# Optimization experiments

Measured on AMD Instinct MI355X. Metric: run time of the kernel, lower is better.

The kernel has to match this reference:

```python
import jax, jax.numpy as jnp
import numpy as np

B, C, N = 8, 128, 2048
HEADS = 4
OUT = 128
HD = OUT // HEADS  # 32


def setup_inputs() -> dict:
    key = jax.random.key(0)
    kx, kq, kk, kv, ko = jax.random.split(key, 5)
    # xavier_uniform bounds
    def xavier(k, shape, fan_in, fan_out):
        a = float(np.sqrt(6.0 / (fan_in + fan_out)))
        return jax.random.uniform(k, shape, jnp.float32, -a, a)
    return {
        "x": jax.random.normal(kx, (B, C, N), jnp.float32),
        "W_q": xavier(kq, (HEADS, C, HD), C, HD),
        "W_k": xavier(kk, (HEADS, C, HD), C, HD),
        "W_v": xavier(kv, (HEADS, C, HD), C, HD),
        "W_o": xavier(ko, (OUT, OUT), OUT, OUT),
    }


def reference(x, W_q, W_k, W_v, W_o):
    # x: [B, C, N] -> x_t: [B, N, C]
    x_t = jnp.transpose(x, (0, 2, 1))
    # per-head projections: [B, H, N, d]
    q = jnp.einsum("bnc,hcd->bhnd", x_t, W_q)
    k = jnp.einsum("bnc,hcd->bhnd", x_t, W_k)
    v = jnp.einsum("bnc,hcd->bhnd", x_t, W_v)
    scale = 1.0 / jnp.sqrt(jnp.asarray(HD, jnp.float32))
    # materialized score matrix [B, H, N, N]
    scores = jax.nn.softmax(jnp.einsum("bhnd,bhmd->bhnm", q, k) * scale, axis=-1)
    # weighted sum per head then concat heads: [B, N, H*d]
    out = jnp.einsum("bhnm,bhmd->bhnd", scores, v)
    out = jnp.transpose(out, (0, 2, 1, 3)).reshape(B, N, OUT)
    out = out @ W_o  # [B, N, OUT]
    adj = jnp.mean(scores, axis=1)  # [B, N, N]
    return jnp.transpose(out, (0, 2, 1)), adj
```

## Files before the change

### kernel.cpp

```cpp
#include <hip/hip_runtime.h>
#include <hip/hip_bf16.h>

#define NB 8
#define NC 128
#define NN 2048
#define NH 4
#define HD 32
#define NOUT 128

typedef _Float16 half8 __attribute__((ext_vector_type(8)));
typedef float f32x4 __attribute__((ext_vector_type(4)));

__device__ __forceinline__ f32x4 mfma16(half8 a, half8 b, f32x4 c) {
  return __builtin_amdgcn_mfma_f32_16x16x32_f16(a, b, c, 0, 0, 0);
}

__global__ __launch_bounds__(256) void k_proj(
    const float* __restrict__ x, const float* __restrict__ Wq,
    const float* __restrict__ Wk, const float* __restrict__ Wv,
    _Float16* __restrict__ qo, _Float16* __restrict__ ko, _Float16* __restrict__ vto)
{
  const int bid = blockIdx.x;
  const int b  = bid & 7;
  const int n0 = (bid >> 3) * 64;
  const int h  = threadIdx.x >> 6;
  const int l  = threadIdx.x & 63;
  const int lr = l & 15, lg = l >> 4;

  half8 a[4][4];
#pragma unroll
  for (int rf = 0; rf < 4; ++rf)
#pragma unroll
    for (int kc = 0; kc < 4; ++kc)
#pragma unroll
      for (int j = 0; j < 8; ++j)
        a[rf][kc][j] = (_Float16)x[(size_t)(b*NC + kc*32 + lg*8 + j)*NN + n0 + rf*16 + lr];

#pragma unroll
  for (int m = 0; m < 2; ++m) {
    const float* W = m ? Wk : Wq;
    _Float16* dst  = m ? ko : qo;
    f32x4 acc[4][2] = {};
#pragma unroll
    for (int kc = 0; kc < 4; ++kc) {
      half8 wb[2];
#pragma unroll
      for (int cf = 0; cf < 2; ++cf)
#pragma unroll
        for (int j = 0; j < 8; ++j)
          wb[cf][j] = (_Float16)W[(size_t)(h*NC + kc*32 + lg*8 + j)*HD + cf*16 + lr];
#pragma unroll
      for (int rf = 0; rf < 4; ++rf)
#pragma unroll
        for (int cf = 0; cf < 2; ++cf)
          acc[rf][cf] = mfma16(a[rf][kc], wb[cf], acc[rf][cf]);
    }
#pragma unroll
    for (int rf = 0; rf < 4; ++rf)
#pragma unroll
      for (int cf = 0; cf < 2; ++cf)
#pragma unroll
        for (int r = 0; r < 4; ++r)
          dst[((size_t)(b*NH + h)*NN + n0 + rf*16 + lg*4 + r)*HD + cf*16 + lr] =
              (_Float16)acc[rf][cf][r];
  }

  {
    half8 aw[2][4];
#pragma unroll
    for (int rf = 0; rf < 2; ++rf)
#pragma unroll
      for (int kc = 0; kc < 4; ++kc)
#pragma unroll
        for (int j = 0; j < 8; ++j)
          aw[rf][kc][j] = (_Float16)Wv[(size_t)(h*NC + kc*32 + lg*8 + j)*HD + rf*16 + lr];
    f32x4 acc[2][4] = {};
#pragma unroll
    for (int kc = 0; kc < 4; ++kc)
#pragma unroll
      for (int rf = 0; rf < 2; ++rf)
#pragma unroll
        for (int nf = 0; nf < 4; ++nf)
          acc[rf][nf] = mfma16(aw[rf][kc], a[nf][kc], acc[rf][nf]);
#pragma unroll
    for (int rf = 0; rf < 2; ++rf)
#pragma unroll
      for (int nf = 0; nf < 4; ++nf)
#pragma unroll
        for (int r = 0; r < 4; ++r)
          vto[((size_t)(b*NH + h)*HD + rf*16 + lg*4 + r)*NN + n0 + nf*16 + lr] =
              (_Float16)acc[rf][nf][r];
  }
}

union SMem {
  _Float16 p[NH * 32 * 72];
  struct { _Float16 ocat[32 * 136]; float ot[128 * 36]; } ep;
};

__global__ __launch_bounds__(256) void k_attn(
    const _Float16* __restrict__ q, const _Float16* __restrict__ k,
    const _Float16* __restrict__ vt, const float* __restrict__ Wo,
    float* __restrict__ outT, float* __restrict__ adj)
{
  __shared__ SMem sm;
  const int bid = blockIdx.x;
  const int b  = bid & 7;
  const int n0 = (bid >> 3) * 32;
  const int h  = threadIdx.x >> 6;
  const int l  = threadIdx.x & 63;
  const int lr = l & 15, lg = l >> 4;

  const _Float16* qh = q  + (size_t)(b*NH + h) * NN * HD;
  const _Float16* kh = k  + (size_t)(b*NH + h) * NN * HD;
  const _Float16* vh = vt + (size_t)(b*NH + h) * HD * NN;

  half8 qa[2];
  qa[0] = *(const half8*)(qh + (size_t)(n0 + lr)*HD + lg*8);
  qa[1] = *(const half8*)(qh + (size_t)(n0 + 16 + lr)*HD + lg*8);

  const float c1 = 0.25504527f;
  const float c2 = 17.3123405f;

  float rs[2][4] = {};
  for (int mt = 0; mt < NN/16; ++mt) {
    half8 kb = *(const half8*)(kh + (size_t)(mt*16 + lr)*HD + lg*8);
    f32x4 z{};
    f32x4 s0 = mfma16(qa[0], kb, z);
    f32x4 s1 = mfma16(qa[1], kb, z);
#pragma unroll
    for (int r = 0; r < 4; ++r) {
      rs[0][r] += __builtin_amdgcn_exp2f(s0[r]*c1 - c2);
      rs[1][r] += __builtin_amdgcn_exp2f(s1[r]*c1 - c2);
    }
  }
#pragma unroll
  for (int rf = 0; rf < 2; ++rf)
#pragma unroll
    for (int r = 0; r < 4; ++r) {
      float v = rs[rf][r];
      v += __shfl_xor(v, 1); v += __shfl_xor(v, 2);
      v += __shfl_xor(v, 4); v += __shfl_xor(v, 8);
      rs[rf][r] = 1.0f / v;
    }

  f32x4 oacc[2][2] = {};
  const int tr = threadIdx.x >> 3;
  const int tc = (threadIdx.x & 7) * 8;

  for (int mt2 = 0; mt2 < NN/64; ++mt2) {
#pragma unroll
    for (int st = 0; st < 4; ++st) {
      half8 kb = *(const half8*)(kh + (size_t)(mt2*64 + st*16 + lr)*HD + lg*8);
      f32x4 z{};
      f32x4 s0 = mfma16(qa[0], kb, z);
      f32x4 s1 = mfma16(qa[1], kb, z);
#pragma unroll
      for (int r = 0; r < 4; ++r) {
        sm.p[h*2304 + (lg*4 + r)*72 + st*16 + lr] =
            (_Float16)(__builtin_amdgcn_exp2f(s0[r]*c1 - c2) * rs[0][r]);
        sm.p[h*2304 + (16 + lg*4 + r)*72 + st*16 + lr] =
            (_Float16)(__builtin_amdgcn_exp2f(s1[r]*c1 - c2) * rs[1][r]);
      }
    }
    __syncthreads();
#pragma unroll
    for (int kc = 0; kc < 2; ++kc) {
      half8 pa0 = *(const half8*)(&sm.p[h*2304 + lr*72 + kc*32 + lg*8]);
      half8 pa1 = *(const half8*)(&sm.p[h*2304 + (16 + lr)*72 + kc*32 + lg*8]);
      half8 vb0 = *(const half8*)(vh + (size_t)lr*NN        + mt2*64 + kc*32 + lg*8);
      half8 vb1 = *(const half8*)(vh + (size_t)(16 + lr)*NN + mt2*64 + kc*32 + lg*8);
      oacc[0][0] = mfma16(pa0, vb0, oacc[0][0]);
      oacc[0][1] = mfma16(pa0, vb1, oacc[0][1]);
      oacc[1][0] = mfma16(pa1, vb0, oacc[1][0]);
      oacc[1][1] = mfma16(pa1, vb1, oacc[1][1]);
    }
    {
      float a8[8] = {};
#pragma unroll
      for (int h2 = 0; h2 < 4; ++h2) {
        half8 pv = *(const half8*)(&sm.p[h2*2304 + tr*72 + tc]);
#pragma unroll
        for (int i = 0; i < 8; ++i) a8[i] += (float)pv[i];
      }
      size_t base = ((size_t)(b*NN) + n0 + tr)*NN + mt2*64 + tc;
      f32x4 w0 = {a8[0]*0.25f, a8[1]*0.25f, a8[2]*0.25f, a8[3]*0.25f};
      f32x4 w1 = {a8[4]*0.25f, a8[5]*0.25f, a8[6]*0.25f, a8[7]*0.25f};
      *(f32x4*)(adj + base)     = w0;
      *(f32x4*)(adj + base + 4) = w1;
    }
    __syncthreads();
  }

#pragma unroll
  for (int rf = 0; rf < 2; ++rf)
#pragma unroll
    for (int df = 0; df < 2; ++df)
#pragma unroll
      for (int r = 0; r < 4; ++r)
        sm.ep.ocat[(rf*16 + lg*4 + r)*136 + h*32 + df*16 + lr] = (_Float16)oacc[rf][df][r];
  __syncthreads();

  f32x4 o2[2][2] = {};
#pragma unroll
  for (int kc = 0; kc < 4; ++kc) {
    half8 a2[2];
    a2[0] = *(const half8*)(&sm.ep.ocat[lr*136        + kc*32 + lg*8]);
    a2[1] = *(const half8*)(&sm.ep.ocat[(16 + lr)*136 + kc*32 + lg*8]);
    half8 wb[2];
#pragma unroll
    for (int of = 0; of < 2; ++of)
#pragma unroll
      for (int j = 0; j < 8; ++j)
        wb[of][j] = (_Float16)Wo[(size_t)(kc*32 + lg*8 + j)*NOUT + h*32 + of*16 + lr];
#pragma unroll
    for (int rf = 0; rf < 2; ++rf)
#pragma unroll
      for (int of = 0; of < 2; ++of)
        o2[rf][of] = mfma16(a2[rf], wb[of], o2[rf][of]);
  }
#pragma unroll
  for (int rf = 0; rf < 2; ++rf)
#pragma unroll
    for (int of = 0; of < 2; ++of)
#pragma unroll
      for (int r = 0; r < 4; ++r)
        sm.ep.ot[(h*32 + of*16 + lr)*36 + rf*16 + lg*4 + r] = o2[rf][of][r];
  __syncthreads();
  {
    int o  = threadIdx.x >> 1;
    int nn = (threadIdx.x & 1) * 16;
    float* dst = outT + ((size_t)(b*NOUT) + o)*NN + n0 + nn;
#pragma unroll
    for (int i = 0; i < 4; ++i)
      *(f32x4*)(dst + i*4) = *(const f32x4*)(&sm.ep.ot[o*36 + nn + i*4]);
  }
}

extern "C" void kernel_launch(void* const* d_in, const int* in_sizes, int n_in,
                              void* d_out, int out_size, void* d_ws, size_t ws_size,
                              hipStream_t stream) {
  const float* x  = (const float*)d_in[0];
  const float* Wq = (const float*)d_in[1];
  const float* Wk = (const float*)d_in[2];
  const float* Wv = (const float*)d_in[3];
  const float* Wo = (const float*)d_in[4];

  float* outT = (float*)d_out;
  float* adj  = outT + (size_t)NB * NOUT * NN;

  const size_t qkv_elems = (size_t)NB * NH * NN * HD;
  _Float16* qw = (_Float16*)d_ws;
  _Float16* kw = qw + qkv_elems;
  _Float16* vw = kw + qkv_elems;

  k_proj<<<dim3(NB * (NN/64)), dim3(256), 0, stream>>>(x, Wq, Wk, Wv, qw, kw, vw);
  k_attn<<<dim3(NB * (NN/32)), dim3(256), 0, stream>>>(qw, kw, vw, Wo, outT, adj);
}
```

Before: 260.0 us.

## Halve attention query tile, pre-transpose weights to fp16, stage x via LDS

The attention kernel now processes 16 query rows per block instead of 32, doubling the grid to 1024 blocks for better occupancy and latency hiding. The cost is that K and V are reread twice as often. A new prep kernel converts and transposes all weight matrices to fp16 once, so the projection and output GEMMs can use vector loads instead of strided scalar converts. The projection kernel also stages x through shared memory with coalesced float4 loads and uses smaller 32-column tiles.

```diff
diff --git a/kernel.cpp b/kernel.cpp
--- a/kernel.cpp
+++ b/kernel.cpp
@@ -7,233 +7,234 @@
 #define NH 4
 #define HD 32
 #define NOUT 128
+#define QB 16
 
 typedef _Float16 half8 __attribute__((ext_vector_type(8)));
+typedef _Float16 half4 __attribute__((ext_vector_type(4)));
 typedef float f32x4 __attribute__((ext_vector_type(4)));
 
 __device__ __forceinline__ f32x4 mfma16(half8 a, half8 b, f32x4 c) {
   return __builtin_amdgcn_mfma_f32_16x16x32_f16(a, b, c, 0, 0, 0);
 }
 
+__global__ __launch_bounds__(256) void k_prep(
+    const float* __restrict__ Wq, const float* __restrict__ Wk,
+    const float* __restrict__ Wv, const float* __restrict__ Wo,
+    _Float16* __restrict__ WqT, _Float16* __restrict__ WkT,
+    _Float16* __restrict__ WvT, _Float16* __restrict__ WoT)
+{
+  int id = blockIdx.x * 256 + threadIdx.x;
+  if (id < 3 * 16384) {
+    int m = id >> 14, rem = id & 16383;
+    int h = rem >> 12, d = (rem >> 7) & 31, c = rem & 127;
+    const float* W = (m == 0) ? Wq : (m == 1) ? Wk : Wv;
+    _Float16* WT   = (m == 0) ? WqT : (m == 1) ? WkT : WvT;
+    WT[(h * 32 + d) * 128 + c] = (_Float16)W[(h * 128 + c) * 32 + d];
+  } else {
+    int j = id - 49152;
+    int o = j >> 7, c = j & 127;
+    WoT[o * 128 + c] = (_Float16)Wo[c * 128 + o];
+  }
+}
+
 __global__ __launch_bounds__(256) void k_proj(
-    const float* __restrict__ x, const float* __restrict__ Wq,
-    const float* __restrict__ Wk, const float* __restrict__ Wv,
+    const float* __restrict__ x, const _Float16* __restrict__ WqT,
+    const _Float16* __restrict__ WkT, const _Float16* __restrict__ WvT,
     _Float16* __restrict__ qo, _Float16* __restrict__ ko, _Float16* __restrict__ vto)
 {
+  __shared__ _Float16 xs[32][136];
   const int bid = blockIdx.x;
   const int b  = bid & 7;
-  const int n0 = (bid >> 3) * 64;
-  const int h  = threadIdx.x >> 6;
-  const int l  = threadIdx.x & 63;
-  const int lr = l & 15, lg = l >> 4;
-
-  half8 a[4][4];
-#pragma unroll
-  for (int rf = 0; rf < 4; ++rf)
+  const int n0 = (bid >> 3) * 32;
+  const int tid = threadIdx.x;
+  const int h = tid >> 6, l = tid & 63, lr = l & 15, lg = l >> 4;
+
+  {
+    int c  = tid >> 1;
+    int nq = (tid & 1) * 16;
+    const float* src = x + (size_t)(b * NC + c) * NN + n0 + nq;
+#pragma unroll
+    for (int i = 0; i < 4; ++i) {
+      f32x4 v = *(const f32x4*)(src + i * 4);
+#pragma unroll
+      for (int j = 0; j < 4; ++j) xs[nq + i * 4 + j][c] = (_Float16)v[j];
+    }
+  }
+  __syncthreads();
+
+  half8 a[2][4];
+#pragma unroll
+  for (int rf = 0; rf < 2; ++rf)
 #pragma unroll
     for (int kc = 0; kc < 4; ++kc)
-#pragma unroll
-      for (int j = 0; j < 8; ++j)
-        a[rf][kc][j] = (_Float16)x[(size_t)(b*NC + kc*32 + lg*8 + j)*NN + n0 + rf*16 + lr];
+      a[rf][kc] = *(const half8*)(&xs[rf * 16 + lr][kc * 32 + lg * 8]);
 
 #pragma unroll
   for (int m = 0; m < 2; ++m) {
-    const float* W = m ? Wk : Wq;
-    _Float16* dst  = m ? ko : qo;
-    f32x4 acc[4][2] = {};
+    const _Float16* WT = m ? WkT : WqT;
+    _Float16* dst      = m ? ko : qo;
+    f32x4 acc[2][2] = {};
 #pragma unroll
     for (int kc = 0; kc < 4; ++kc) {
       half8 wb[2];
 #pragma unroll
       for (int cf = 0; cf < 2; ++cf)
-#pragma unroll
-        for (int j = 0; j < 8; ++j)
-          wb[cf][j] = (_Float16)W[(size_t)(h*NC + kc*32 + lg*8 + j)*HD + cf*16 + lr];
-#pragma unroll
-      for (int rf = 0; rf < 4; ++rf)
+        wb[cf] = *(const half8*)(WT + (size_t)(h * HD + cf * 16 + lr) * NC + kc * 32 + lg * 8);
+#pragma unroll
+      for (int rf = 0; rf < 2; ++rf)
 #pragma unroll
         for (int cf = 0; cf < 2; ++cf)
           acc[rf][cf] = mfma16(a[rf][kc], wb[cf], acc[rf][cf]);
     }
 #pragma unroll
-    for (int rf = 0; rf < 4; ++rf)
+    for (int rf = 0; rf < 2; ++rf)
 #pragma unroll
       for (int cf = 0; cf < 2; ++cf)
 #pragma unroll
         for (int r = 0; r < 4; ++r)
-          dst[((size_t)(b*NH + h)*NN + n0 + rf*16 + lg*4 + r)*HD + cf*16 + lr] =
+          dst[((size_t)(b * NH + h) * NN + n0 + rf * 16 + lg * 4 + r) * HD + cf * 16 + lr] =
               (_Float16)acc[rf][cf][r];
   }
 
   {
-    half8 aw[2][4];
+    f32x4 acc[2][2] = {};
+#pragma unroll
+    for (int kc = 0; kc < 4; ++kc) {
+      half8 aw[2];
+#pragma unroll
+      for (int rf = 0; rf < 2; ++rf)
+        aw[rf] = *(const half8*)(WvT + (size_t)(h * HD + rf * 16 + lr) * NC + kc * 32 + lg * 8);
+#pragma unroll
+      for (int rf = 0; rf < 2; ++rf)
+#pragma unroll
+        for (int nf = 0; nf < 2; ++nf)
+          acc[rf][nf] = mfma16(aw[rf], a[nf][kc], acc[rf][nf]);
+    }
 #pragma unroll
     for (int rf = 0; rf < 2; ++rf)
 #pragma unroll
-      for (int kc = 0; kc < 4; ++kc)
-#pragma unroll
-        for (int j = 0; j < 8; ++j)
-          aw[rf][kc][j] = (_Float16)Wv[(size_t)(h*NC + kc*32 + lg*8 + j)*HD + rf*16 + lr];
-    f32x4 acc[2][4] = {};
-#pragma unroll
-    for (int kc = 0; kc < 4; ++kc)
-#pragma unroll
-      for (int rf = 0; rf < 2; ++rf)
-#pragma unroll
-        for (int nf = 0; nf < 4; ++nf)
-          acc[rf][nf] = mfma16(aw[rf][kc], a[nf][kc], acc[rf][nf]);
-#pragma unroll
-    for (int rf = 0; rf < 2; ++rf)
-#pragma unroll
-      for (int nf = 0; nf < 4; ++nf)
+      for (int nf = 0; nf < 2; ++nf)
 #pragma unroll
         for (int r = 0; r < 4; ++r)
-          vto[((size_t)(b*NH + h)*HD + rf*16 + lg*4 + r)*NN + n0 + nf*16 + lr] =
+          vto[((size_t)(b * NH + h) * HD + rf * 16 + lg * 4 + r) * NN + n0 + nf * 16 + lr] =
               (_Float16)acc[rf][nf][r];
   }
 }
 
 union SMem {
-  _Float16 p[NH * 32 * 72];
-  struct { _Float16 ocat[32 * 136]; float ot[128 * 36]; } ep;
+  _Float16 p[NH * QB * 72];
+  struct { _Float16 ocat[QB * 136]; float ot[128 * 20]; } ep;
 };
 
 __global__ __launch_bounds__(256) void k_attn(
     const _Float16* __restrict__ q, const _Float16* __restrict__ k,
-    const _Float16* __restrict__ vt, const float* __restrict__ Wo,
+    const _Float16* __restrict__ vt, const _Float16* __restrict__ WoT,
     float* __restrict__ outT, float* __restrict__ adj)
 {
   __shared__ SMem sm;
   const int bid = blockIdx.x;
   const int b  = bid & 7;
-  const int n0 = (bid >> 3) * 32;
+  const int n0 = (bid >> 3) * QB;
   const int h  = threadIdx.x >> 6;
   const int l  = threadIdx.x & 63;
   const int lr = l & 15, lg = l >> 4;
 
-  const _Float16* qh = q  + (size_t)(b*NH + h) * NN * HD;
-  const _Float16* kh = k  + (size_t)(b*NH + h) * NN * HD;
-  const _Float16* vh = vt + (size_t)(b*NH + h) * HD * NN;
-
-  half8 qa[2];
-  qa[0] = *(const half8*)(qh + (size_t)(n0 + lr)*HD + lg*8);
-  qa[1] = *(const half8*)(qh + (size_t)(n0 + 16 + lr)*HD + lg*8);
+  const _Float16* qh = q  + (size_t)(b * NH + h) * NN * HD;
+  const _Float16* kh = k  + (size_t)(b * NH + h) * NN * HD;
+  const _Float16* vh = vt + (size_t)(b * NH + h) * HD * NN;
+
+  half8 qa = *(const half8*)(qh + (size_t)(n0 + lr) * HD + lg * 8);
 
   const float c1 = 0.25504527f;
   const float c2 = 17.3123405f;
 
-  float rs[2][4] = {};
-  for (int mt = 0; mt < NN/16; ++mt) {
-    half8 kb = *(const half8*)(kh + (size_t)(mt*16 + lr)*HD + lg*8);
+  float rs[4] = {};
+  for (int mt = 0; mt < NN / 32; ++mt) {
+    half8 kb0 = *(const half8*)(kh + (size_t)(mt * 32 + lr) * HD + lg * 8);
+    half8 kb1 = *(const half8*)(kh + (size_t)(mt * 32 + 16 + lr) * HD + lg * 8);
     f32x4 z{};
-    f32x4 s0 = mfma16(qa[0], kb, z);
-    f32x4 s1 = mfma16(qa[1], kb, z);
-#pragma unroll
-    for (int r = 0; r < 4; ++r) {
-      rs[0][r] += __builtin_amdgcn_exp2f(s0[r]*c1 - c2);
-      rs[1][r] += __builtin_amdgcn_exp2f(s1[r]*c1 - c2);
-    }
-  }
-#pragma unroll
-  for (int rf = 0; rf < 2; ++rf)
-#pragma unroll
-    for (int r = 0; r < 4; ++r) {
-      float v = rs[rf][r];
-      v += __shfl_xor(v, 1); v += __shfl_xor(v, 2);
-      v += __shfl_xor(v, 4); v += __shfl_xor(v, 8);
-      rs[rf][r] = 1.0f / v;
-    }
-
-  f32x4 oacc[2][2] = {};
-  const int tr = threadIdx.x >> 3;
-  const int tc = (threadIdx.x & 7) * 8;
-
-  for (int mt2 = 0; mt2 < NN/64; ++mt2) {
+    f32x4 s0 = mfma16(qa, kb0, z);
+    f32x4 s1 = mfma16(qa, kb1, z);
+#pragma unroll
+    for (int r = 0; r < 4; ++r)
+      rs[r] += __builtin_amdgcn_exp2f(s0[r] * c1 - c2) +
+               __builtin_amdgcn_exp2f(s1[r] * c1 - c2);
+  }
+#pragma unroll
+  for (int r = 0; r < 4; ++r) {
+    float v = rs[r];
+    v += __shfl_xor(v, 1); v += __shfl_xor(v, 2);
+    v += __shfl_xor(v, 4); v += __shfl_xor(v, 8);
+    rs[r] = 1.0f / v;
+  }
+
+  f32x4 oacc[2] = {};
+  const int tr = threadIdx.x >> 4;
+  const int tc = (threadIdx.x & 15) * 4;
+
+  for (int mt2 = 0; mt2 < NN / 64; ++mt2) {
 #pragma unroll
     for (int st = 0; st < 4; ++st) {
-      half8 kb = *(const half8*)(kh + (size_t)(mt2*64 + st*16 + lr)*HD + lg*8);
+      half8 kb = *(const half8*)(kh + (size_t)(mt2 * 64 + st * 16 + lr) * HD + lg * 8);
       f32x4 z{};
-      f32x4 s0 = mfma16(qa[0], kb, z);
-      f32x4 s1 = mfma16(qa[1], kb, z);
-#pragma unroll
-      for (int r = 0; r < 4; ++r) {
-        sm.p[h*2304 + (lg*4 + r)*72 + st*16 + lr] =
-            (_Float16)(__builtin_amdgcn_exp2f(s0[r]*c1 - c2) * rs[0][r]);
-        sm.p[h*2304 + (16 + lg*4 + r)*72 + st*16 + lr] =
-            (_Float16)(__builtin_amdgcn_exp2f(s1[r]*c1 - c2) * rs[1][r]);
+      f32x4 s = mfma16(qa, kb, z);
+#pragma unroll
+      for (int r = 0; r < 4; ++r)
+        sm.p[(h * QB + lg * 4 + r) * 72 + st * 16 + lr] =
+            (_Float16)(__builtin_amdgcn_exp2f(s[r] * c1 - c2) * rs[r]);
+    }
+    __syncthreads();
+#pragma unroll
+    for (int kc = 0; kc < 2; ++kc) {
+      half8 pa  = *(const half8*)(&sm.p[(h * QB + lr) * 72 + kc * 32 + lg * 8]);
+      half8 vb0 = *(const half8*)(vh + (size_t)lr * NN        + mt2 * 64 + kc * 32 + lg * 8);
+      half8 vb1 = *(const half8*)(vh + (size_t)(16 + lr) * NN + mt2 * 64 + kc * 32 + lg * 8);
+      oacc[0] = mfma16(pa, vb0, oacc[0]);
+      oacc[1] = mfma16(pa, vb1, oacc[1]);
+    }
+    {
+      float a4[4] = {};
+#pragma unroll
+      for (int h2 = 0; h2 < 4; ++h2) {
+        half4 pv = *(const half4*)(&sm.p[(h2 * QB + tr) * 72 + tc]);
+#pragma unroll
+        for (int i = 0; i < 4; ++i) a4[i] += (float)pv[i];
       }
+      f32x4 w = {a4[0] * 0.25f, a4[1] * 0.25f, a4[2] * 0.25f, a4[3] * 0.25f};
+      *(f32x4*)(adj + ((size_t)(b * NN) + n0 + tr) * NN + mt2 * 64 + tc) = w;
     }
     __syncthreads();
-#pragma unroll
-    for (int kc = 0; kc < 2; ++kc) {
-      half8 pa0 = *(const half8*)(&sm.p[h*2304 + lr*72 + kc*32 + lg*8]);
-      half8 pa1 = *(const half8*)(&sm.p[h*2304 + (16 + lr)*72 + kc*32 + lg*8]);
-      half8 vb0 = *(const half8*)(vh + (size_t)lr*NN        + mt2*64 + kc*32 + lg*8);
-      half8 vb1 = *(const half8*)(vh + (size_t)(16 + lr)*NN + mt2*64 + kc*32 + lg*8);
-      oacc[0][0] = mfma16(pa0, vb0, oacc[0][0]);
-      oacc[0][1] = mfma16(pa0, vb1, oacc[0][1]);
-      oacc[1][0] = mfma16(pa1, vb0, oacc[1][0]);
-      oacc[1][1] = mfma16(pa1, vb1, oacc[1][1]);
-    }
-    {
-      float a8[8] = {};
-#pragma unroll
-      for (int h2 = 0; h2 < 4; ++h2) {
-        half8 pv = *(const half8*)(&sm.p[h2*2304 + tr*72 + tc]);
-#pragma unroll
-        for (int i = 0; i < 8; ++i) a8[i] += (float)pv[i];
-      }
-      size_t base = ((size_t)(b*NN) + n0 + tr)*NN + mt2*64 + tc;
-      f32x4 w0 = {a8[0]*0.25f, a8[1]*0.25f, a8[2]*0.25f, a8[3]*0.25f};
-      f32x4 w1 = {a8[4]*0.25f, a8[5]*0.25f, a8[6]*0.25f, a8[7]*0.25f};
-      *(f32x4*)(adj + base)     = w0;
-      *(f32x4*)(adj + base + 4) = w1;
-    }
-    __syncthreads();
-  }
-
-#pragma unroll
-  for (int rf = 0; rf < 2; ++rf)
-#pragma unroll
-    for (int df = 0; df < 2; ++df)
-#pragma unroll
-      for (int r = 0; r < 4; ++r)
-        sm.ep.ocat[(rf*16 + lg*4 + r)*136 + h*32 + df*16 + lr] = (_Float16)oacc[rf][df][r];
+  }
+
+#pragma unroll
+  for (int df = 0; df < 2; ++df)
+#pragma unroll
+    for (int r = 0; r < 4; ++r)
+      sm.ep.ocat[(lg * 4 + r) * 136 + h * 32 + df * 16 + lr] = (_Float16)oacc[df][r];
   __syncthreads();
 
-  f32x4 o2[2][2] = {};
+  f32x4 o2[2] = {};
 #pragma unroll
   for (int kc = 0; kc < 4; ++kc) {
-    half8 a2[2];
-    a2[0] = *(const half8*)(&sm.ep.ocat[lr*136        + kc*32 + lg*8]);
-    a2[1] = *(const half8*)(&sm.ep.ocat[(16 + lr)*136 + kc*32 + lg*8]);
-    half8 wb[2];
-#pragma unroll
-    for (int of = 0; of < 2; ++of)
-#pragma unroll
-      for (int j = 0; j < 8; ++j)
-        wb[of][j] = (_Float16)Wo[(size_t)(kc*32 + lg*8 + j)*NOUT + h*32 + of*16 + lr];
-#pragma unroll
-    for (int rf = 0; rf < 2; ++rf)
-#pragma unroll
-      for (int of = 0; of < 2; ++of)
-        o2[rf][of] = mfma16(a2[rf], wb[of], o2[rf][of]);
-  }
-#pragma unroll
-  for (int rf = 0; rf < 2; ++rf)
-#pragma unroll
-    for (int of = 0; of < 2; ++of)
-#pragma unroll
-      for (int r = 0; r < 4; ++r)
-        sm.ep.ot[(h*32 + of*16 + lr)*36 + rf*16 + lg*4 + r] = o2[rf][of][r];
+    half8 a2 = *(const half8*)(&sm.ep.ocat[lr * 136 + kc * 32 + lg * 8]);
+#pragma unroll
+    for (int of = 0; of < 2; ++of) {
+      half8 wb = *(const half8*)(WoT + (size_t)(h * 32 + of * 16 + lr) * NOUT + kc * 32 + lg * 8);
+      o2[of] = mfma16(a2, wb, o2[of]);
+    }
+  }
+#pragma unroll
+  for (int of = 0; of < 2; ++of)
+#pragma unroll
+    for (int r = 0; r < 4; ++r)
+      sm.ep.ot[(h * 32 + of * 16 + lr) * 20 + lg * 4 + r] = o2[of][r];
   __syncthreads();
   {
     int o  = threadIdx.x >> 1;
-    int nn = (threadIdx.x & 1) * 16;
-    float* dst = outT + ((size_t)(b*NOUT) + o)*NN + n0 + nn;
-#pragma unroll
-    for (int i = 0; i < 4; ++i)
-      *(f32x4*)(dst + i*4) = *(const f32x4*)(&sm.ep.ot[o*36 + nn + i*4]);
+    int hf = threadIdx.x & 1;
+    float* dst = outT + ((size_t)(b * NOUT) + o) * NN + n0 + hf * 8;
+    *(f32x4*)(dst)     = *(const f32x4*)(&sm.ep.ot[o * 20 + hf * 8]);
+    *(f32x4*)(dst + 4) = *(const f32x4*)(&sm.ep.ot[o * 20 + hf * 8 + 4]);
   }
 }
 
@@ -250,10 +251,15 @@
   float* adj  = outT + (size_t)NB * NOUT * NN;
 
   const size_t qkv_elems = (size_t)NB * NH * NN * HD;
-  _Float16* qw = (_Float16*)d_ws;
-  _Float16* kw = qw + qkv_elems;
-  _Float16* vw = kw + qkv_elems;
-
-  k_proj<<<dim3(NB * (NN/64)), dim3(256), 0, stream>>>(x, Wq, Wk, Wv, qw, kw, vw);
-  k_attn<<<dim3(NB * (NN/32)), dim3(256), 0, stream>>>(qw, kw, vw, Wo, outT, adj);
-}
+  _Float16* qw  = (_Float16*)d_ws;
+  _Float16* kw  = qw + qkv_elems;
+  _Float16* vw  = kw + qkv_elems;
+  _Float16* wqT = vw + qkv_elems;
+  _Float16* wkT = wqT + 16384;
+  _Float16* wvT = wkT + 16384;
+  _Float16* woT = wvT + 16384;
+
+  k_prep<<<dim3(256), dim3(256), 0, stream>>>(Wq, Wk, Wv, Wo, wqT, wkT, wvT, woT);
+  k_proj<<<dim3(NB * (NN / 32)), dim3(256), 0, stream>>>(x, wqT, wkT, wvT, qw, kw, vw);
+  k_attn<<<dim3(NB * (NN / QB)), dim3(256), 0, stream>>>(qw, kw, vw, woT, outT, adj);
+}
```

New measurement: 267.1 us. 1.03x slower.
